# Kernel optimization log

Hardware: AMD Instinct MI355X
Metric: run time of the kernel (lower is better)

The kernel has to match this reference:

```python
import jax, jax.numpy as jnp
import numpy as np
import math

B, H, S, D = 2, 16, 2048, 64

def setup_inputs() -> dict:
    key = jax.random.key(0)
    k1, k2, k3, k4 = jax.random.split(key, 4)
    query = jax.random.normal(k1, (B, H, S, D), dtype=jnp.float32)
    key_t = jax.random.normal(k2, (B, H, S, D), dtype=jnp.float32)
    value = jax.random.normal(k3, (B, H, S, D), dtype=jnp.float32)
    mask = jax.random.randint(k4, (B, 1, 1, S), 0, 2).astype(bool)
    return {"query": query, "key": key_t, "value": value, "mask": mask}

def reference(query, key, value, mask):
    model_dim = query.shape[-1]
    q = query / jnp.asarray(math.sqrt(model_dim), query.dtype)
    # scores: [B,H,S,S]
    scores = jnp.einsum('bhqd,bhkd->bhqk', q, key)
    masking_value = -1e30 if scores.dtype == jnp.float32 else -10000.0
    scores = jnp.where(mask, jnp.asarray(masking_value, scores.dtype), scores)
    attention = jax.nn.softmax(scores, axis=-1)
    sum_value = jnp.einsum('bhqk,bhkd->bhqd', attention, value)
    return (attention, sum_value)
```

## Files before the change

kernel.cpp:

```cpp
#include <hip/hip_runtime.h>
#include <stdint.h>


#define S_DIM 2048
#define D_DIM 64
#define QT 32
#define KTILE 64
#define NKT 32
#define NT 512
#define NBH 32
#define ETS 72
#define ATTN_ELEMS ((size_t)NBH * S_DIM * S_DIM)
#define QELEMS ((size_t)NBH * S_DIM * D_DIM)

typedef short s16x8 __attribute__((ext_vector_type(8)));
typedef float f32x4 __attribute__((ext_vector_type(4)));

__device__ __forceinline__ unsigned short f2bf(float x) {
  unsigned int u = __float_as_uint(x);
  u += 0x7FFF + ((u >> 16) & 1);
  return (unsigned short)(u >> 16);
}
__device__ __forceinline__ float bf2f(unsigned short h) {
  return __uint_as_float(((unsigned int)h) << 16);
}

__device__ __forceinline__ void glds16(const void* g, void* l) {
  __builtin_amdgcn_global_load_lds(
      (const __attribute__((address_space(1))) unsigned int*)g,
      (__attribute__((address_space(3))) unsigned int*)l, 16, 0, 0);
}

extern "C" __global__ __launch_bounds__(256)
void prep_kernel(const float* __restrict__ Q, const float* __restrict__ K,
                 const float* __restrict__ V, unsigned short* __restrict__ Qb,
                 unsigned short* __restrict__ Kb, unsigned short* __restrict__ Vtb) {
  __shared__ unsigned short vtl[64 * 65];
  const int t = threadIdx.x;
  const int blk = blockIdx.x;
  if (blk < 1024) {
    const int bh = blk >> 5;
    const int kt = blk & 31;
    const float* Ksrc = K + ((size_t)bh * S_DIM + kt * KTILE) * D_DIM;
    const float* Vsrc = V + ((size_t)bh * S_DIM + kt * KTILE) * D_DIM;
    unsigned short* Kdst = Kb + ((size_t)bh * S_DIM + kt * KTILE) * D_DIM;
    unsigned short* Vdst = Vtb + ((size_t)bh * S_DIM + kt * KTILE) * D_DIM;
#pragma unroll
    for (int i = 0; i < 2; ++i) {
      const int f = t + i * 256;
      const int row = f >> 3, db = f & 7;
      const float* s = Ksrc + row * 64 + db * 8;
      s16x8 v;
#pragma unroll
      for (int j = 0; j < 8; ++j) v[j] = (short)f2bf(s[j]);
      *(s16x8*)(Kdst + row * 64 + ((db * 8) ^ ((row & 7) * 8))) = v;
    }
#pragma unroll
    for (int i = 0; i < 4; ++i) {
      const int f = t + i * 256;
      const int row = f >> 4, c4 = f & 15;
      const float4 vv = *(const float4*)(Vsrc + row * 64 + c4 * 4);
      vtl[(c4 * 4 + 0) * 65 + row] = f2bf(vv.x);
      vtl[(c4 * 4 + 1) * 65 + row] = f2bf(vv.y);
      vtl[(c4 * 4 + 2) * 65 + row] = f2bf(vv.z);
      vtl[(c4 * 4 + 3) * 65 + row] = f2bf(vv.w);
    }
    __syncthreads();
#pragma unroll
    for (int i = 0; i < 2; ++i) {
      const int f = t + i * 256;
      const int d = f >> 3, b8 = f & 7;
      s16x8 v;
#pragma unroll
      for (int j = 0; j < 8; ++j) v[j] = (short)vtl[d * 65 + b8 * 8 + j];
      *(s16x8*)(Vdst + d * 64 + ((b8 * 8) ^ ((d & 7) * 8))) = v;
    }
  } else {
    const size_t base = (size_t)(blk - 1024) * 2048 + (size_t)t * 8;
    const float4 a = *(const float4*)(Q + base);
    const float4 b2 = *(const float4*)(Q + base + 4);
    s16x8 v;
    v[0] = (short)f2bf(a.x * 0.125f);  v[1] = (short)f2bf(a.y * 0.125f);
    v[2] = (short)f2bf(a.z * 0.125f);  v[3] = (short)f2bf(a.w * 0.125f);
    v[4] = (short)f2bf(b2.x * 0.125f); v[5] = (short)f2bf(b2.y * 0.125f);
    v[6] = (short)f2bf(b2.z * 0.125f); v[7] = (short)f2bf(b2.w * 0.125f);
    *(s16x8*)(Qb + base) = v;
  }
}

extern "C" __global__ __launch_bounds__(NT, 4)
void attn_kernel(const int* __restrict__ Mask, const unsigned short* __restrict__ Qb,
                 const unsigned short* __restrict__ Kb, const unsigned short* __restrict__ Vtb,
                 float* __restrict__ Out) {
  __shared__ unsigned short bufK[2][KTILE * D_DIM];
  __shared__ unsigned short bufV[2][KTILE * D_DIM];
  __shared__ unsigned short et[QT * ETS];
  __shared__ float sums_part[8 * 16];
  __shared__ float inv_sums[QT];

  const int t = threadIdx.x;
  const int lane = t & 63;
  const int wave = t >> 6;
  const int l15 = lane & 15;
  const int quad = lane >> 4;
  const int tq = wave >> 2;
  const int tn = wave & 3;

  const int blk0 = blockIdx.x;
  const int blk = (blk0 & 7) * 256 + (blk0 >> 3);
  const int qt_idx = blk & 63;
  const int bh = blk >> 6;
  const int q0 = qt_idx * QT;

  const char* kbase = (const char*)(Kb + (size_t)bh * S_DIM * D_DIM);
  const char* vbase = (const char*)(Vtb + (size_t)bh * S_DIM * D_DIM);
  const int* mrow = Mask + (bh >> 4) * S_DIM + tn * 16 + l15;

  const unsigned short* qrow = Qb + ((size_t)bh * S_DIM + q0 + tq * 16 + l15) * D_DIM;
  const s16x8 qf0 = *(const s16x8*)(qrow + quad * 8);
  const s16x8 qf1 = *(const s16x8*)(qrow + 32 + quad * 8);

  glds16(kbase + t * 16, (char*)bufK[0] + wave * 1024);
  glds16(vbase + t * 16, (char*)bufV[0] + wave * 1024);

  f32x4 pv = {0.f, 0.f, 0.f, 0.f};
  float rs[4] = {0.f, 0.f, 0.f, 0.f};
  unsigned int ereg[NKT][2];

  const int krow = tn * 16 + l15;
  const int sw = (l15 & 7) * 8;
  const int erow0 = tq * 16 + quad * 4;

#pragma unroll
  for (int kt = 0; kt < NKT; ++kt) {
    const int p = kt & 1;
    __syncthreads();
    if (kt + 1 < NKT) {
      glds16(kbase + (size_t)(kt + 1) * 8192 + t * 16, (char*)bufK[1 - p] + wave * 1024);
      glds16(vbase + (size_t)(kt + 1) * 8192 + t * 16, (char*)bufV[1 - p] + wave * 1024);
    }
    const int m = mrow[kt * KTILE];
    const unsigned short* kb = bufK[p];
    f32x4 sc = {0.f, 0.f, 0.f, 0.f};
    {
      const s16x8 b0 = *(const s16x8*)(kb + krow * 64 + ((quad * 8) ^ sw));
      sc = __builtin_amdgcn_mfma_f32_16x16x32_bf16(qf0, b0, sc, 0, 0, 0);
      const s16x8 b1 = *(const s16x8*)(kb + krow * 64 + ((32 + quad * 8) ^ sw));
      sc = __builtin_amdgcn_mfma_f32_16x16x32_bf16(qf1, b1, sc, 0, 0, 0);
    }
    unsigned short e[4];
#pragma unroll
    for (int r = 0; r < 4; ++r) {
      const float ev = m ? 0.f : __expf(sc[r]);
      e[r] = f2bf(ev);
      rs[r] += bf2f(e[r]);
      et[(erow0 + r) * ETS + tn * 16 + l15] = e[r];
    }
    ereg[kt][0] = (unsigned int)e[0] | ((unsigned int)e[1] << 16);
    ereg[kt][1] = (unsigned int)e[2] | ((unsigned int)e[3] << 16);
    __builtin_amdgcn_sched_barrier(0);
    asm volatile("s_waitcnt lgkmcnt(0)" ::: "memory");
    __builtin_amdgcn_s_barrier();
    __builtin_amdgcn_sched_barrier(0);
    const unsigned short* vb = bufV[p];
    {
      const s16x8 a0 = *(const s16x8*)(et + (tq * 16 + l15) * ETS + quad * 8);
      const s16x8 b0 = *(const s16x8*)(vb + krow * 64 + ((quad * 8) ^ sw));
      pv = __builtin_amdgcn_mfma_f32_16x16x32_bf16(a0, b0, pv, 0, 0, 0);
      const s16x8 a1 = *(const s16x8*)(et + (tq * 16 + l15) * ETS + 32 + quad * 8);
      const s16x8 b1 = *(const s16x8*)(vb + krow * 64 + ((32 + quad * 8) ^ sw));
      pv = __builtin_amdgcn_mfma_f32_16x16x32_bf16(a1, b1, pv, 0, 0, 0);
    }
  }

#pragma unroll
  for (int o = 1; o < 16; o <<= 1) {
#pragma unroll
    for (int r = 0; r < 4; ++r) rs[r] += __shfl_xor(rs[r], o);
  }
  if (l15 == 0) {
#pragma unroll
    for (int r = 0; r < 4; ++r) sums_part[wave * 16 + quad * 4 + r] = rs[r];
  }
  __syncthreads();
  if (t < QT) {
    const int tqi = t >> 4, rl = t & 15;
    float s = 0.f;
#pragma unroll
    for (int w = 0; w < 4; ++w) s += sums_part[(tqi * 4 + w) * 16 + rl];
    inv_sums[t] = 1.f / fmaxf(s, 1e-30f);
  }
  __syncthreads();

  float inv_r[4];
#pragma unroll
  for (int r = 0; r < 4; ++r) inv_r[r] = inv_sums[erow0 + r];

  {
    float* svo = Out + ATTN_ELEMS + ((size_t)bh * S_DIM + q0) * D_DIM;
#pragma unroll
    for (int r = 0; r < 4; ++r)
      __builtin_nontemporal_store(pv[r] * inv_r[r],
                                  svo + (size_t)(erow0 + r) * D_DIM + tn * 16 + l15);
  }

  float* ao = Out + (size_t)bh * S_DIM * S_DIM + (size_t)q0 * S_DIM + tn * 16 + l15;
#pragma unroll
  for (int kt = 0; kt < NKT; ++kt) {
    float* col = ao + kt * KTILE;
    __builtin_nontemporal_store(bf2f((unsigned short)(ereg[kt][0] & 0xFFFFu)) * inv_r[0],
                                col + (size_t)(erow0 + 0) * S_DIM);
    __builtin_nontemporal_store(bf2f((unsigned short)(ereg[kt][0] >> 16)) * inv_r[1],
                                col + (size_t)(erow0 + 1) * S_DIM);
    __builtin_nontemporal_store(bf2f((unsigned short)(ereg[kt][1] & 0xFFFFu)) * inv_r[2],
                                col + (size_t)(erow0 + 2) * S_DIM);
    __builtin_nontemporal_store(bf2f((unsigned short)(ereg[kt][1] >> 16)) * inv_r[3],
                                col + (size_t)(erow0 + 3) * S_DIM);
  }
}

extern "C" void kernel_launch(void* const* d_in, const int* in_sizes, int n_in,
                              void* d_out, int out_size, void* d_ws, size_t ws_size,
                              hipStream_t stream) {
  const float* Q = (const float*)d_in[0];
  const float* K = (const float*)d_in[1];
  const float* V = (const float*)d_in[2];
  const int* M = (const int*)d_in[3];
  float* out = (float*)d_out;
  unsigned short* Qb = (unsigned short*)d_ws;
  unsigned short* Kb = Qb + QELEMS;
  unsigned short* Vtb = Kb + QELEMS;
  hipLaunchKernelGGL(prep_kernel, dim3(3072), dim3(256), 0, stream, Q, K, V, Qb, Kb, Vtb);
  hipLaunchKernelGGL(attn_kernel, dim3(2048), dim3(NT), 0, stream, M, Qb, Kb, Vtb, out);
}
```

Measured before the change: 737.8 us.

## Split attention into two passes with direct register K/V loads and streamed stores

Drops the LDS double-buffered K/V staging and loads K and V fragments straight from global memory into registers, with a three-deep register prefetch. The kernel now makes two passes: the first computes only the row sums, and the second recomputes the scores, writes the normalized attention tile by tile, and accumulates P·V. This frees the large per-thread ereg array and lets the attention stores overlap with compute. In exchange it doubles the QK MFMA and exp work and re-reads K from L2, and the per-lane global loads may be less coalesced than the previous LDS path.

Result: slower. 783.4 us (+6.2%).

```diff
diff --git a/kernel.cpp b/kernel.cpp
--- a/kernel.cpp
+++ b/kernel.cpp
@@ -23,12 +23,6 @@
 }
 __device__ __forceinline__ float bf2f(unsigned short h) {
   return __uint_as_float(((unsigned int)h) << 16);
-}
-
-__device__ __forceinline__ void glds16(const void* g, void* l) {
-  __builtin_amdgcn_global_load_lds(
-      (const __attribute__((address_space(1))) unsigned int*)g,
-      (__attribute__((address_space(3))) unsigned int*)l, 16, 0, 0);
 }
 
 extern "C" __global__ __launch_bounds__(256)
@@ -92,9 +86,7 @@
 void attn_kernel(const int* __restrict__ Mask, const unsigned short* __restrict__ Qb,
                  const unsigned short* __restrict__ Kb, const unsigned short* __restrict__ Vtb,
                  float* __restrict__ Out) {
-  __shared__ unsigned short bufK[2][KTILE * D_DIM];
-  __shared__ unsigned short bufV[2][KTILE * D_DIM];
-  __shared__ unsigned short et[QT * ETS];
+  __shared__ unsigned short et[2][QT * ETS];
   __shared__ float sums_part[8 * 16];
   __shared__ float inv_sums[QT];
 
@@ -112,64 +104,51 @@
   const int bh = blk >> 6;
   const int q0 = qt_idx * QT;
 
-  const char* kbase = (const char*)(Kb + (size_t)bh * S_DIM * D_DIM);
-  const char* vbase = (const char*)(Vtb + (size_t)bh * S_DIM * D_DIM);
-  const int* mrow = Mask + (bh >> 4) * S_DIM + tn * 16 + l15;
+  const unsigned short* kbg = Kb + (size_t)bh * S_DIM * D_DIM;
+  const unsigned short* vbg = Vtb + (size_t)bh * S_DIM * D_DIM;
 
   const unsigned short* qrow = Qb + ((size_t)bh * S_DIM + q0 + tq * 16 + l15) * D_DIM;
   const s16x8 qf0 = *(const s16x8*)(qrow + quad * 8);
   const s16x8 qf1 = *(const s16x8*)(qrow + 32 + quad * 8);
 
-  glds16(kbase + t * 16, (char*)bufK[0] + wave * 1024);
-  glds16(vbase + t * 16, (char*)bufV[0] + wave * 1024);
-
-  f32x4 pv = {0.f, 0.f, 0.f, 0.f};
-  float rs[4] = {0.f, 0.f, 0.f, 0.f};
-  unsigned int ereg[NKT][2];
-
   const int krow = tn * 16 + l15;
   const int sw = (l15 & 7) * 8;
+  const int o0 = (quad * 8) ^ sw;
+  const int o1 = (32 + quad * 8) ^ sw;
+  const unsigned short* kR = kbg + krow * 64;
+  const unsigned short* vR = vbg + krow * 64;
+
+  const int* mrow = Mask + (bh >> 4) * S_DIM + tn * 16 + l15;
+  unsigned pm = 0;
+#pragma unroll
+  for (int kt = 0; kt < NKT; ++kt) pm |= (mrow[kt * KTILE] ? 1u : 0u) << kt;
+
   const int erow0 = tq * 16 + quad * 4;
 
-#pragma unroll
-  for (int kt = 0; kt < NKT; ++kt) {
-    const int p = kt & 1;
-    __syncthreads();
-    if (kt + 1 < NKT) {
-      glds16(kbase + (size_t)(kt + 1) * 8192 + t * 16, (char*)bufK[1 - p] + wave * 1024);
-      glds16(vbase + (size_t)(kt + 1) * 8192 + t * 16, (char*)bufV[1 - p] + wave * 1024);
-    }
-    const int m = mrow[kt * KTILE];
-    const unsigned short* kb = bufK[p];
-    f32x4 sc = {0.f, 0.f, 0.f, 0.f};
-    {
-      const s16x8 b0 = *(const s16x8*)(kb + krow * 64 + ((quad * 8) ^ sw));
-      sc = __builtin_amdgcn_mfma_f32_16x16x32_bf16(qf0, b0, sc, 0, 0, 0);
-      const s16x8 b1 = *(const s16x8*)(kb + krow * 64 + ((32 + quad * 8) ^ sw));
-      sc = __builtin_amdgcn_mfma_f32_16x16x32_bf16(qf1, b1, sc, 0, 0, 0);
-    }
-    unsigned short e[4];
-#pragma unroll
-    for (int r = 0; r < 4; ++r) {
-      const float ev = m ? 0.f : __expf(sc[r]);
-      e[r] = f2bf(ev);
-      rs[r] += bf2f(e[r]);
-      et[(erow0 + r) * ETS + tn * 16 + l15] = e[r];
-    }
-    ereg[kt][0] = (unsigned int)e[0] | ((unsigned int)e[1] << 16);
-    ereg[kt][1] = (unsigned int)e[2] | ((unsigned int)e[3] << 16);
-    __builtin_amdgcn_sched_barrier(0);
-    asm volatile("s_waitcnt lgkmcnt(0)" ::: "memory");
-    __builtin_amdgcn_s_barrier();
-    __builtin_amdgcn_sched_barrier(0);
-    const unsigned short* vb = bufV[p];
-    {
-      const s16x8 a0 = *(const s16x8*)(et + (tq * 16 + l15) * ETS + quad * 8);
-      const s16x8 b0 = *(const s16x8*)(vb + krow * 64 + ((quad * 8) ^ sw));
-      pv = __builtin_amdgcn_mfma_f32_16x16x32_bf16(a0, b0, pv, 0, 0, 0);
-      const s16x8 a1 = *(const s16x8*)(et + (tq * 16 + l15) * ETS + 32 + quad * 8);
-      const s16x8 b1 = *(const s16x8*)(vb + krow * 64 + ((32 + quad * 8) ^ sw));
-      pv = __builtin_amdgcn_mfma_f32_16x16x32_bf16(a1, b1, pv, 0, 0, 0);
+  float rs[4] = {0.f, 0.f, 0.f, 0.f};
+  {
+    s16x8 kf0[3], kf1[3];
+    kf0[0] = *(const s16x8*)(kR + o0);
+    kf1[0] = *(const s16x8*)(kR + o1);
+    kf0[1] = *(const s16x8*)(kR + 4096 + o0);
+    kf1[1] = *(const s16x8*)(kR + 4096 + o1);
+#pragma unroll
+    for (int kt = 0; kt < NKT; ++kt) {
+      const int cur = kt % 3;
+      if (kt + 2 < NKT) {
+        const int nx = (kt + 2) % 3;
+        kf0[nx] = *(const s16x8*)(kR + (kt + 2) * 4096 + o0);
+        kf1[nx] = *(const s16x8*)(kR + (kt + 2) * 4096 + o1);
+      }
+      f32x4 sc = {0.f, 0.f, 0.f, 0.f};
+      sc = __builtin_amdgcn_mfma_f32_16x16x32_bf16(qf0, kf0[cur], sc, 0, 0, 0);
+      sc = __builtin_amdgcn_mfma_f32_16x16x32_bf16(qf1, kf1[cur], sc, 0, 0, 0);
+      const int m = (pm >> kt) & 1;
+#pragma unroll
+      for (int r = 0; r < 4; ++r) {
+        const float ev = m ? 0.f : __expf(sc[r]);
+        rs[r] += bf2f(f2bf(ev));
+      }
     }
   }
 
@@ -196,26 +175,64 @@
 #pragma unroll
   for (int r = 0; r < 4; ++r) inv_r[r] = inv_sums[erow0 + r];
 
+  f32x4 pv = {0.f, 0.f, 0.f, 0.f};
+  float* ao = Out + (size_t)bh * S_DIM * S_DIM + (size_t)q0 * S_DIM + tn * 16 + l15;
+  {
+    s16x8 kf0[3], kf1[3], vf0[3], vf1[3];
+    kf0[0] = *(const s16x8*)(kR + o0);
+    kf1[0] = *(const s16x8*)(kR + o1);
+    vf0[0] = *(const s16x8*)(vR + o0);
+    vf1[0] = *(const s16x8*)(vR + o1);
+    kf0[1] = *(const s16x8*)(kR + 4096 + o0);
+    kf1[1] = *(const s16x8*)(kR + 4096 + o1);
+    vf0[1] = *(const s16x8*)(vR + 4096 + o0);
+    vf1[1] = *(const s16x8*)(vR + 4096 + o1);
+#pragma unroll
+    for (int kt = 0; kt < NKT; ++kt) {
+      const int cur = kt % 3;
+      if (kt + 2 < NKT) {
+        const int nx = (kt + 2) % 3;
+        kf0[nx] = *(const s16x8*)(kR + (kt + 2) * 4096 + o0);
+        kf1[nx] = *(const s16x8*)(kR + (kt + 2) * 4096 + o1);
+        vf0[nx] = *(const s16x8*)(vR + (kt + 2) * 4096 + o0);
+        vf1[nx] = *(const s16x8*)(vR + (kt + 2) * 4096 + o1);
+      }
+      f32x4 sc = {0.f, 0.f, 0.f, 0.f};
+      sc = __builtin_amdgcn_mfma_f32_16x16x32_bf16(qf0, kf0[cur], sc, 0, 0, 0);
+      sc = __builtin_amdgcn_mfma_f32_16x16x32_bf16(qf1, kf1[cur], sc, 0, 0, 0);
+      const int m = (pm >> kt) & 1;
+      unsigned short* etp = et[kt & 1];
+      unsigned short e[4];
+#pragma unroll
+      for (int r = 0; r < 4; ++r) {
+        const float ev = m ? 0.f : __expf(sc[r]);
+        e[r] = f2bf(ev);
+        etp[(erow0 + r) * ETS + tn * 16 + l15] = e[r];
+      }
+      float* col = ao + kt * KTILE;
+      __builtin_nontemporal_store(bf2f(e[0]) * inv_r[0], col + (size_t)(erow0 + 0) * S_DIM);
+      __builtin_nontemporal_store(bf2f(e[1]) * inv_r[1], col + (size_t)(erow0 + 1) * S_DIM);
+      __builtin_nontemporal_store(bf2f(e[2]) * inv_r[2], col + (size_t)(erow0 + 2) * S_DIM);
+      __builtin_nontemporal_store(bf2f(e[3]) * inv_r[3], col + (size_t)(erow0 + 3) * S_DIM);
+      __builtin_amdgcn_sched_barrier(0);
+      asm volatile("s_waitcnt lgkmcnt(0)" ::: "memory");
+      __builtin_amdgcn_s_barrier();
+      __builtin_amdgcn_sched_barrier(0);
+      {
+        const s16x8 a0 = *(const s16x8*)(etp + (tq * 16 + l15) * ETS + quad * 8);
+        pv = __builtin_amdgcn_mfma_f32_16x16x32_bf16(a0, vf0[cur], pv, 0, 0, 0);
+        const s16x8 a1 = *(const s16x8*)(etp + (tq * 16 + l15) * ETS + 32 + quad * 8);
+        pv = __builtin_amdgcn_mfma_f32_16x16x32_bf16(a1, vf1[cur], pv, 0, 0, 0);
+      }
+    }
+  }
+
   {
     float* svo = Out + ATTN_ELEMS + ((size_t)bh * S_DIM + q0) * D_DIM;
 #pragma unroll
     for (int r = 0; r < 4; ++r)
       __builtin_nontemporal_store(pv[r] * inv_r[r],
                                   svo + (size_t)(erow0 + r) * D_DIM + tn * 16 + l15);
-  }
-
-  float* ao = Out + (size_t)bh * S_DIM * S_DIM + (size_t)q0 * S_DIM + tn * 16 + l15;
-#pragma unroll
-  for (int kt = 0; kt < NKT; ++kt) {
-    float* col = ao + kt * KTILE;
-    __builtin_nontemporal_store(bf2f((unsigned short)(ereg[kt][0] & 0xFFFFu)) * inv_r[0],
-                                col + (size_t)(erow0 + 0) * S_DIM);
-    __builtin_nontemporal_store(bf2f((unsigned short)(ereg[kt][0] >> 16)) * inv_r[1],
-                                col + (size_t)(erow0 + 1) * S_DIM);
-    __builtin_nontemporal_store(bf2f((unsigned short)(ereg[kt][1] & 0xFFFFu)) * inv_r[2],
-                                col + (size_t)(erow0 + 2) * S_DIM);
-    __builtin_nontemporal_store(bf2f((unsigned short)(ereg[kt][1] >> 16)) * inv_r[3],
-                                col + (size_t)(erow0 + 3) * S_DIM);
   }
 }
 
```
